# Kernel optimization log

Hardware: AMD Instinct MI355X
Metric: run time of the kernel (lower is better)

## Reference

```python
import jax, jax.numpy as jnp
import numpy as np

TEMP = 0.1
EPS = 1e-12  # F.normalize eps


def setup_inputs() -> dict:
    key = jax.random.key(0)
    k1, k2 = jax.random.split(key)
    B, C, N = 8, 128, 4096
    features = jax.random.normal(k1, (B, C, N), dtype=jnp.float32)
    labels_all = jax.random.randint(k2, (B, N), 0, 16, dtype=jnp.int32)
    return {"features": features, "labels_all": labels_all}


def _per_cloud_loss(features_map, labels):
    # features_map: [C, N], labels: [N]
    v = features_map.T  # [N, C]
    v = v / jnp.maximum(jnp.linalg.norm(v, axis=1, keepdims=True), EPS)
    dp = jnp.exp(jnp.matmul(v, v.T) / TEMP)  # [N, N]
    n = dp.shape[0]
    # remove diagonal (dot_products - diag(diagonal))
    dp = dp * (1.0 - jnp.eye(n, dtype=dp.dtype))
    mask = labels[:, None] == labels[None, :]  # [N, N]
    positives = jnp.sum(jnp.where(mask, dp, 0.0), axis=1)
    negatives = jnp.sum(jnp.where(mask, 0.0, dp), axis=1)
    deviation = -jnp.log(positives / (positives + negatives))
    return jnp.mean(deviation)


def reference(features, labels_all):
    # features: [B, C, N], labels_all: [B, N]
    losses = jax.vmap(_per_cloud_loss)(features, labels_all)  # [B]
    return jnp.mean(losses)
```

## Files before the change

### kernel.cpp

```cpp
#include <hip/hip_runtime.h>
#include <hip/hip_bf16.h>
#include <math.h>

#define BATCH 8
#define NPTS 4096
#define CH 128
#define CTG 8
#define ROWS 128
#define CHUNK 32
#define NCHUNK (NPTS / (CTG * CHUNK))
#define NBUF 6

#define SQRT_TEMP_LOG2E 3.79828256f

typedef __attribute__((ext_vector_type(4))) float    f32x4;
typedef __attribute__((ext_vector_type(4))) int      i32x4;
typedef __attribute__((ext_vector_type(8))) short    bf16x8;
typedef __attribute__((ext_vector_type(4))) _Float16 f16x4;

typedef __attribute__((address_space(3))) unsigned int lds_uint;
typedef __attribute__((address_space(1))) const unsigned int gbl_uint;

__device__ __forceinline__ void load_lds16(const void* g, const void* l) {
    __builtin_amdgcn_global_load_lds((gbl_uint*)g, (lds_uint*)l, 16, 0, 0);
}

__device__ __forceinline__ float fast_exp2(float x) {
    return __builtin_amdgcn_exp2f(x);
}

__device__ __forceinline__ f32x4 mfma16(f16x4 a, f16x4 b, f32x4 c) {
#if __has_builtin(__builtin_amdgcn_mfma_f32_16x16x16f16)
    return __builtin_amdgcn_mfma_f32_16x16x16f16(a, b, c, 0, 0, 0);
#else
    f32x4 d = c;
    asm volatile("v_mfma_f32_16x16x16_f16 %0, %1, %2, %0"
                 : "+v"(d) : "v"(a), "v"(b));
    return d;
#endif
}

__global__ __launch_bounds__(256) void normalize_kernel(
    const float* __restrict__ f, __hip_bfloat16* __restrict__ vn,
    float* __restrict__ pos, float* __restrict__ neg, float* __restrict__ out)
{
    const int blk = blockIdx.x;
    const int b = blk >> 6;
    const int n0 = (blk & 63) * 64;
    const int nl = threadIdx.x & 63;
    const int cg = threadIdx.x >> 6;
    const float* base = f + (size_t)b * CH * NPTS + (size_t)(cg * 32) * NPTS
                          + n0 + nl;

    __shared__ float red[4][64];
    __shared__ float scl[64];
    __shared__ short ostage[64 * CH];

    float ss = 0.0f;
    #pragma unroll
    for (int c = 0; c < 32; c++) {
        float v = base[(size_t)c * NPTS];
        ss += v * v;
    }
    red[cg][nl] = ss;
    __syncthreads();
    if (cg == 0) {
        float s = red[0][nl] + red[1][nl] + red[2][nl] + red[3][nl];
        scl[nl] = SQRT_TEMP_LOG2E / fmaxf(sqrtf(s), 1e-12f);
    }
    __syncthreads();
    const float scale = scl[nl];

    #pragma unroll
    for (int k = 0; k < 4; k++) {
        union { __hip_bfloat16 h[8]; uint4 u; } pk;
        #pragma unroll
        for (int j = 0; j < 8; j++) {
            float v = base[(size_t)(k * 8 + j) * NPTS] * scale;
            pk.h[j] = __float2bfloat16(v);
        }
        const int ch8 = cg * 4 + k;
        const int phys = (nl << 4) | (ch8 ^ (nl & 15));
        *(uint4*)&ostage[phys * 8] = pk.u;
    }
    __syncthreads();

    __hip_bfloat16* ob = vn + ((size_t)b * NPTS + n0) * CH;
    const int t = threadIdx.x;
    #pragma unroll
    for (int it = 0; it < 4; it++) {
        const int L = it * 256 + t;
        const int pt = L >> 4, c8 = L & 15;
        const int phys = (pt << 4) | (c8 ^ (pt & 15));
        *(uint4*)(ob + (size_t)L * 8) = *(const uint4*)&ostage[phys * 8];
    }

    if (cg == 0) pos[b * NPTS + n0 + nl] = 0.0f;
    else if (cg == 1) neg[b * NPTS + n0 + nl] = 0.0f;
    if (blk == 0 && t == 0) out[0] = 0.0f;
}

__global__ __launch_bounds__(256, 4) void tile_kernel(
    const __hip_bfloat16* __restrict__ vn, const int* __restrict__ labels,
    float* __restrict__ pos, float* __restrict__ neg)
{
    __shared__ short lB[NBUF][CHUNK * CH];
    __shared__ int labL[NPTS / CTG];

    const int ctg = blockIdx.x, rt = blockIdx.y, b = blockIdx.z;
    const int tid = threadIdx.x;
    const int w = tid >> 6, lane = tid & 63;
    const int lane15 = lane & 15, quad = lane >> 4;

    const int row0 = rt * ROWS;
    const int colbase = ctg * (NPTS / CTG);
    const __hip_bfloat16* vb = vn + (size_t)b * NPTS * CH;
    const int* labb = labels + b * NPTS;

    auto stage = [&](int buf, int chunk) {
        const __hip_bfloat16* Bb = vb + (size_t)(colbase + chunk * CHUNK) * CH;
        #pragma unroll
        for (int i = 0; i < 2; i++) {
            int ldsrow = w * 8 + i * 4;
            int r = ldsrow + quad;
            int g = lane15 ^ (r & 15);
            load_lds16(Bb + (size_t)r * CH + g * 8, &lB[buf][ldsrow * CH]);
        }
    };

    load_lds16(labb + colbase + (w & 1) * 256 + lane * 4, &labL[(w & 1) * 256]);

    bf16x8 afrag[2][4];
    int lr[2];
    #pragma unroll
    for (int mi = 0; mi < 2; mi++) {
        const int row_l = w * 32 + mi * 16 + lane15;
        const __hip_bfloat16* Arow = vb + (size_t)(row0 + row_l) * CH;
        #pragma unroll
        for (int ks = 0; ks < 4; ks++)
            afrag[mi][ks] = *(const bf16x8*)(Arow + (ks * 4 + quad) * 8);
        lr[mi] = labb[row0 + row_l];
    }

    stage(0, 0);
    stage(1, 1);
    stage(2, 2);
    stage(3, 3);

    int vad[2][4];
    #pragma unroll
    for (int ni = 0; ni < 2; ni++)
        #pragma unroll
        for (int ks = 0; ks < 4; ks++)
            vad[ni][ks] = (((ni * 16 + lane15) * CH) +
                           (((ks * 4 + quad) ^ lane15) << 3)) * 2;

    f32x4 qout[2] = {{0.0f, 0.0f, 0.0f, 0.0f}, {0.0f, 0.0f, 0.0f, 0.0f}};
    float ddiag[2] = {0.0f, 0.0f};
    const f32x4 zf = {0.0f, 0.0f, 0.0f, 0.0f};
    f32x4 accA[2][2], accB[2][2];

#define MFMA_PH(BUF_, ACC_)                                                   \
    {                                                                         \
        _Pragma("unroll")                                                     \
        for (int ni = 0; ni < 2; ni++) {                                      \
            bf16x8 bf = *(const bf16x8*)((const char*)(&lB[0][0]) +           \
                         (BUF_) * (CHUNK * CH * 2) + vad[ni][0]);             \
            ACC_[0][ni] = __builtin_amdgcn_mfma_f32_16x16x32_bf16(            \
                bf, afrag[0][0], zf, 0, 0, 0);                                \
            ACC_[1][ni] = __builtin_amdgcn_mfma_f32_16x16x32_bf16(            \
                bf, afrag[1][0], zf, 0, 0, 0);                                \
        }                                                                     \
        _Pragma("unroll")                                                     \
        for (int ks = 1; ks < 4; ks++) {                                      \
            _Pragma("unroll")                                                 \
            for (int ni = 0; ni < 2; ni++) {                                  \
                bf16x8 bf = *(const bf16x8*)((const char*)(&lB[0][0]) +       \
                             (BUF_) * (CHUNK * CH * 2) + vad[ni][ks]);        \
                ACC_[0][ni] = __builtin_amdgcn_mfma_f32_16x16x32_bf16(        \
                    bf, afrag[0][ks], ACC_[0][ni], 0, 0, 0);                  \
                ACC_[1][ni] = __builtin_amdgcn_mfma_f32_16x16x32_bf16(        \
                    bf, afrag[1][ks], ACC_[1][ni], 0, 0, 0);                  \
            }                                                                 \
        }                                                                     \
    }

#define EPI_PH(EC_, ACC_)                                                     \
    {                                                                         \
        _Pragma("unroll")                                                     \
        for (int ni = 0; ni < 2; ni++) {                                      \
            const i32x4 lc = *(const i32x4*)&labL[(EC_) * CHUNK + ni * 16 +   \
                                                  quad * 4];                  \
            f16x4 oh;                                                         \
            _Pragma("unroll")                                                 \
            for (int j = 0; j < 4; j++)                                       \
                oh[j] = (lc[j] == lane15) ? (_Float16)1.0f : (_Float16)0.0f;  \
            const int colblk = colbase + (EC_) * CHUNK + ni * 16;             \
            _Pragma("unroll")                                                 \
            for (int mi = 0; mi < 2; mi++) {                                  \
                f16x4 eh;                                                     \
                _Pragma("unroll")                                             \
                for (int r = 0; r < 4; r++)                                   \
                    eh[r] = (_Float16)fast_exp2(ACC_[mi][ni][r]);             \
                if (colblk == row0 + w * 32 + mi * 16) {    \
                    _Pragma("unroll")                                         \
                    for (int r = 0; r < 4; r++)                               \
                        if (lane15 == quad * 4 + r)                           \
                            ddiag[mi] += (float)eh[r];                        \
                }                                                             \
                qout[mi] = mfma16(oh, eh, qout[mi]);                          \
            }                                                                 \
        }                                                                     \
    }

#define PBODY(P_, BA_, BB_, DOEPI_)                                           \
    {                                                                         \
        __builtin_amdgcn_s_barrier();                                         \
        __builtin_amdgcn_s_setprio(1);                                        \
        MFMA_PH(BA_, accA);                                                   \
        __builtin_amdgcn_s_setprio(0);                                        \
        if (DOEPI_) { EPI_PH(2 * (P_) - 1, accB); }                           \
        __builtin_amdgcn_s_setprio(1);                                        \
        MFMA_PH(BB_, accB);                                                   \
        __builtin_amdgcn_s_setprio(0);                                        \
        stage(((BA_) + 4) % 6, (2 * (P_) + 4) & (NCHUNK - 1));                \
        stage(((BB_) + 4) % 6, (2 * (P_) + 5) & (NCHUNK - 1));                \
        EPI_PH(2 * (P_), accA);                                               \
        asm volatile("s_waitcnt vmcnt(4)" ::: "memory");                      \
    }

    asm volatile("s_waitcnt vmcnt(4)" ::: "memory");
    PBODY(0, 0, 1, 0);
    #pragma unroll 1
    for (int p = 1; p <= 4; p += 3) {
        PBODY(p + 0, 2, 3, 1);
        PBODY(p + 1, 4, 5, 1);
        PBODY(p + 2, 0, 1, 1);
    }
    PBODY(7, 2, 3, 1);
    EPI_PH(15, accB);

#undef PBODY
#undef EPI_PH
#undef MFMA_PH

    #pragma unroll
    for (int mi = 0; mi < 2; mi++) {
        float p = -ddiag[mi], tt = -ddiag[mi];
        #pragma unroll
        for (int r = 0; r < 4; r++) {
            float v = qout[mi][r];
            tt += v;
            p  += (quad * 4 + r == lr[mi]) ? v : 0.0f;
        }
        p  += __shfl_xor(p, 16);   p  += __shfl_xor(p, 32);
        tt += __shfl_xor(tt, 16);  tt += __shfl_xor(tt, 32);
        if (lane < 16) {
            const int row_l = w * 32 + mi * 16 + lane15;
            atomicAdd(&pos[b * NPTS + row0 + row_l], p);
            atomicAdd(&neg[b * NPTS + row0 + row_l], tt - p);
        }
    }
}

__global__ __launch_bounds__(256) void finalize_kernel(
    const float* __restrict__ pos, const float* __restrict__ neg,
    float* __restrict__ out)
{
    int base = blockIdx.x * 1024 + threadIdx.x;
    float acc = 0.0f;
    #pragma unroll
    for (int k = 0; k < 4; k++) {
        int i = base + k * 256;
        float p = pos[i];
        float t = p + neg[i];
        acc += __logf(t / p);
    }
    #pragma unroll
    for (int off = 32; off; off >>= 1) acc += __shfl_down(acc, off);
    __shared__ float red[4];
    if ((threadIdx.x & 63) == 0) red[threadIdx.x >> 6] = acc;
    __syncthreads();
    if (threadIdx.x == 0) {
        float v = red[0] + red[1] + red[2] + red[3];
        atomicAdd(out, v * (1.0f / (BATCH * NPTS)));
    }
}

extern "C" void kernel_launch(void* const* d_in, const int* in_sizes, int n_in,
                              void* d_out, int out_size, void* d_ws, size_t ws_size,
                              hipStream_t stream)
{
    const float* features = (const float*)d_in[0];
    const int*   labels   = (const int*)d_in[1];
    float*       out      = (float*)d_out;

    __hip_bfloat16* vn = (__hip_bfloat16*)d_ws;
    float* pos = (float*)((char*)d_ws + (size_t)BATCH * NPTS * CH * sizeof(__hip_bfloat16));
    float* neg = pos + BATCH * NPTS;

    hipLaunchKernelGGL(normalize_kernel, dim3(512), dim3(256), 0, stream,
                       features, vn, pos, neg, out);
    hipLaunchKernelGGL(tile_kernel, dim3(CTG, NPTS / ROWS, BATCH), dim3(256), 0, stream,
                       vn, labels, pos, neg);
    hipLaunchKernelGGL(finalize_kernel, dim3(32), dim3(256), 0, stream, pos, neg, out);
}
```

Before: 113.2 us.

## Halve column groups per block and rework to single-chunk triple-buffered pipeline

Each block now covers twice as many columns (CTG 8→4), so there are half as many blocks and half as many atomic partial writes, and each block runs longer. The software pipeline changes from a double-chunk body with six LDS buffers to a one-chunk body with three buffers. Each body runs the MFMA for chunk c, issues the stage for chunk c+2, then does the exp epilogue for chunk c-1. This cuts LDS use and may raise occupancy, but it shortens the prefetch distance and lowers grid-level parallelism.

```diff
diff --git a/kernel.cpp b/kernel.cpp
--- a/kernel.cpp
+++ b/kernel.cpp
@@ -5,11 +5,11 @@
 #define BATCH 8
 #define NPTS 4096
 #define CH 128
-#define CTG 8
+#define CTG 4
 #define ROWS 128
 #define CHUNK 32
 #define NCHUNK (NPTS / (CTG * CHUNK))
-#define NBUF 6
+#define NBUF 3
 
 #define SQRT_TEMP_LOG2E 3.79828256f
 
@@ -128,7 +128,7 @@
         }
     };
 
-    load_lds16(labb + colbase + (w & 1) * 256 + lane * 4, &labL[(w & 1) * 256]);
+    load_lds16(labb + colbase + w * 256 + lane * 4, &labL[w * 256]);
 
     bf16x8 afrag[2][4];
     int lr[2];
@@ -144,8 +144,6 @@
 
     stage(0, 0);
     stage(1, 1);
-    stage(2, 2);
-    stage(3, 3);
 
     int vad[2][4];
     #pragma unroll
@@ -213,34 +211,36 @@
         }                                                                     \
     }
 
-#define PBODY(P_, BA_, BB_, DOEPI_)                                           \
+#define BODY(C_, BUF_, CUR_, PRV_, DOEPI_)                                    \
     {                                                                         \
         __builtin_amdgcn_s_barrier();                                         \
         __builtin_amdgcn_s_setprio(1);                                        \
-        MFMA_PH(BA_, accA);                                                   \
+        MFMA_PH(BUF_, CUR_);                                                  \
         __builtin_amdgcn_s_setprio(0);                                        \
-        if (DOEPI_) { EPI_PH(2 * (P_) - 1, accB); }                           \
-        __builtin_amdgcn_s_setprio(1);                                        \
-        MFMA_PH(BB_, accB);                                                   \
-        __builtin_amdgcn_s_setprio(0);                                        \
-        stage(((BA_) + 4) % 6, (2 * (P_) + 4) & (NCHUNK - 1));                \
-        stage(((BB_) + 4) % 6, (2 * (P_) + 5) & (NCHUNK - 1));                \
-        EPI_PH(2 * (P_), accA);                                               \
-        asm volatile("s_waitcnt vmcnt(4)" ::: "memory");                      \
-    }
-
-    asm volatile("s_waitcnt vmcnt(4)" ::: "memory");
-    PBODY(0, 0, 1, 0);
+        stage(((BUF_) + 2) % 3, ((C_) + 2) & (NCHUNK - 1));                   \
+        if (DOEPI_) { EPI_PH((C_) - 1, PRV_); }                               \
+        asm volatile("s_waitcnt vmcnt(2)" ::: "memory");                      \
+    }
+
+    asm volatile("s_waitcnt vmcnt(2)" ::: "memory");
+    BODY(0, 0, accA, accB, 0);
     #pragma unroll 1
-    for (int p = 1; p <= 4; p += 3) {
-        PBODY(p + 0, 2, 3, 1);
-        PBODY(p + 1, 4, 5, 1);
-        PBODY(p + 2, 0, 1, 1);
-    }
-    PBODY(7, 2, 3, 1);
-    EPI_PH(15, accB);
-
-#undef PBODY
+    for (int c = 1; c <= 25; c += 6) {
+        BODY(c + 0, 1, accB, accA, 1);
+        BODY(c + 1, 2, accA, accB, 1);
+        BODY(c + 2, 0, accB, accA, 1);
+        BODY(c + 3, 1, accA, accB, 1);
+        BODY(c + 4, 2, accB, accA, 1);
+        BODY(c + 5, 0, accA, accB, 1);
+    }
+    __builtin_amdgcn_s_barrier();
+    __builtin_amdgcn_s_setprio(1);
+    MFMA_PH(1, accB);
+    __builtin_amdgcn_s_setprio(0);
+    EPI_PH(30, accA);
+    EPI_PH(31, accB);
+
+#undef BODY
 #undef EPI_PH
 #undef MFMA_PH
 
```

Result: faster. 110.6 us (-2.3%).
